# Kernel optimization log

Hardware: AMD Instinct MI355X
Metric: run time of the kernel (lower is better)

Reference implementation:

```python
import jax, jax.numpy as jnp
import numpy as np

_EPS = 1e-5
RC = 5.0   # cutoff radius
L = 20     # number of radial basis functions
N = 10000  # nodes
E = 100000 # edges
F = 128    # in_feats


def _ssp(x):
    # ShiftedSoftplus: softplus(x) - log(2)
    return jax.nn.softplus(x) - jnp.log(2.0)


def _rbf(r):
    # DimeNet radial basis: sqrt(2/rc) * sin(n*pi*r/rc) / r, n = 1..L.  r: [E,1] -> [E,L]
    n = jnp.arange(1, L + 1, dtype=r.dtype)
    return jnp.sqrt(2.0 / RC) * jnp.sin(n * jnp.pi * r / RC) / r


def _fc(u):
    # cosine cutoff applied elementwise: 0.5*(cos(pi*u/rc)+1) for u < rc else 0
    return jnp.where(u < RC, 0.5 * (jnp.cos(jnp.pi * u / RC) + 1.0), 0.0)


def setup_inputs() -> dict:
    key = jax.random.key(0)
    ks = jax.random.split(key, 12)

    def nrm(k, shape, scale=1.0):
        return jax.random.normal(k, shape, dtype=jnp.float32) * scale

    return {
        "x": nrm(ks[0], (N, 3)) * 3.0,           # atomic positions
        "v": nrm(ks[1], (N, F, 3)),               # vector node features
        "s": nrm(ks[2], (N, F)),                  # scalar node features
        "ms1_w": nrm(ks[3], (F, F), F ** -0.5),
        "ms1_b": jnp.zeros((F,), jnp.float32),
        "ms2_w": nrm(ks[4], (3 * F, F), F ** -0.5),
        "ms2_b": jnp.zeros((3 * F,), jnp.float32),
        "mv_w": nrm(ks[5], (3 * F, L), L ** -0.5),
        "mv_b": jnp.zeros((3 * F,), jnp.float32),
        "us1_w": nrm(ks[6], (F, F), F ** -0.5),
        "us1_b": jnp.zeros((F,), jnp.float32),
        "us2_w": nrm(ks[7], (3 * F, F), F ** -0.5),
        "us2_b": jnp.zeros((3 * F,), jnp.float32),
        "src": jax.random.randint(ks[8], (E,), 0, N, dtype=jnp.int32),
        "dst": jax.random.randint(ks[9], (E,), 0, N, dtype=jnp.int32),
    }


def reference(x, v, s, ms1_w, ms1_b, ms2_w, ms2_b, mv_w, mv_b,
              us1_w, us1_b, us2_w, us2_b, src, dst):
    # ---------- pass 1: message1 + reduce1 (sum over incoming edges) ----------
    sj = s[src]                                   # [E,F]   src scalar features
    vj = v[src]                                   # [E,F,3] src vector features
    vec = x[src] - x[dst]                         # [E,3]   x_i - x_j (molecule branch)
    r = jnp.sqrt(jnp.sum(vec ** 2, axis=-1) + _EPS)[:, None]          # [E,1]
    phi = _ssp(sj @ ms1_w.T + ms1_b) @ ms2_w.T + ms2_b                 # [E,3F]
    w = _fc(_rbf(r) @ mv_w.T + mv_b)                                    # [E,3F]
    v_, s_, r_ = jnp.split(phi * w, 3, axis=-1)                         # each [E,F]
    dv_e = vj * v_[:, :, None] + r_[:, :, None] * (vec / r)[:, None, :] # [E,F,3]
    dv = jax.ops.segment_sum(dv_e, dst, num_segments=N)                 # [N,F,3]
    ds = jax.ops.segment_sum(s_, dst, num_segments=N)                   # [N,F]
    v_new = v + dv
    s_new = s + ds

    # ---------- pass 2: message2 + reduce2 (mean over incoming edges) ----------
    s2 = _ssp(s_new[src] @ us1_w.T + us1_b) @ us2_w.T + us2_b           # [E,3F]
    deg = jax.ops.segment_sum(jnp.ones((E,), s.dtype), dst, num_segments=N)
    denom = jnp.maximum(deg, 1.0)
    s_mean = jax.ops.segment_sum(s2, dst, num_segments=N) / denom[:, None]        # [N,3F]
    uv = jax.ops.segment_sum(v_new[src], dst, num_segments=N) / denom[:, None, None]  # [N,F,3]
    avv, asv, ass = jnp.split(s_mean, 3, axis=-1)                       # each [N,F]
    norm = jnp.sqrt(jnp.sum(uv ** 2, axis=-1) + _EPS)[..., None]        # [N,F,1]
    dv2 = uv * avv[:, :, None]                                           # [N,F,3]
    ds2 = jnp.sum((uv / norm) ** 2, axis=-1) * asv + ass                 # [N,F]
    return (v_new + dv2, s_new + ds2)
```

## Files before the change

### kernel.cpp

```cpp
#include <hip/hip_runtime.h>
#include <hip/hip_bf16.h>


#define F_DIM   128
#define F3_DIM  384
#define L_DIM   20
#define CAP     64
#define BATCH   16

typedef __attribute__((ext_vector_type(8))) short short8;
typedef __attribute__((ext_vector_type(4))) float f32x4;
typedef __attribute__((ext_vector_type(4))) unsigned short us4;

struct u3 { unsigned a, b, c; };

__device__ __forceinline__ unsigned short f2bf(float f) {
  union { float f; unsigned u; } a; a.f = f;
  unsigned u = a.u;
  u = (u + 0x7FFFu + ((u >> 16) & 1u)) >> 16;
  return (unsigned short)u;
}
__device__ __forceinline__ float bf2f(unsigned short u) {
  union { unsigned u; float f; } a; a.u = ((unsigned)u) << 16;
  return a.f;
}

__global__ __launch_bounds__(256) void cast_fill_kernel(
    const float* __restrict__ ms1_w, unsigned short* __restrict__ w_ms1,
    const float* __restrict__ ms2_w, unsigned short* __restrict__ w_ms2,
    const float* __restrict__ us1_w, unsigned short* __restrict__ w_us1,
    const float* __restrict__ us2_w, unsigned short* __restrict__ w_us2,
    const float* __restrict__ s,     unsigned short* __restrict__ sbf,
    const float* __restrict__ v,     us4* __restrict__ v4,
    const float* __restrict__ mv_w,  unsigned short* __restrict__ mvwB,
    const int* __restrict__ src, const int* __restrict__ dst,
    int* __restrict__ cursor, int* __restrict__ jbuf,
    unsigned short* __restrict__ c1pad, unsigned short* __restrict__ c2pad,
    int nF, int E)
{
  int i = blockIdx.x * 256 + threadIdx.x;
  if (i < 16384) w_ms1[i] = f2bf(ms1_w[i]);
  if (i < 49152) w_ms2[i] = f2bf(ms2_w[i]);
  if (i < 16384) w_us1[i] = f2bf(us1_w[i]);
  if (i < 49152) w_us2[i] = f2bf(us2_w[i]);
  if (i < nF)    sbf[i] = f2bf(s[i]);
  if (i < nF) {
    const float* vp = v + (size_t)i * 3;
    us4 o; o.x = f2bf(vp[0]); o.y = f2bf(vp[1]); o.z = f2bf(vp[2]); o.w = 0;
    v4[i] = o;
  }
  if (i < 384 * 32) {
    int o = i >> 5, k = i & 31;
    float val = (k < 20) ? mv_w[o * 20 + k] * 0.6324555320336759f : 0.f;
    mvwB[i] = f2bf(val);
  }
  if (i < 768) {
    c1pad[i] = 0;
    c2pad[i] = 0;
  }
  if (i < E) {
    int d = dst[i];
    int p = atomicAdd(&cursor[d], 1);
    if (p < CAP) jbuf[d * CAP + p] = src[i];
  }
}

__global__ __launch_bounds__(512) void mlp_kernel(
    const unsigned short* __restrict__ X,
    const unsigned short* __restrict__ W1,
    const float* __restrict__ B1,
    const unsigned short* __restrict__ W2,
    const float* __restrict__ B2,
    const us4* __restrict__ Vin,
    unsigned short* __restrict__ Yc)
{
  __shared__ float HT[128 * 17];
  const int lane = threadIdx.x & 63;
  const int wave = threadIdx.x >> 6;
  const int c    = lane & 15;
  const int quad = lane >> 4;
  const int m0   = blockIdx.x * 16;

  f32x4 acc = (f32x4){0.f, 0.f, 0.f, 0.f};
#pragma unroll
  for (int kk = 0; kk < 4; kk++) {
    short8 a = *(const short8*)(X + (size_t)(m0 + c) * 128 + kk * 32 + quad * 8);
    short8 b = *(const short8*)(W1 + (size_t)(wave * 16 + c) * 128 + kk * 32 + quad * 8);
    acc = __builtin_amdgcn_mfma_f32_16x16x32_bf16(a, b, acc, 0, 0, 0);
  }
  {
    int k = wave * 16 + c;
    float bias = B1[k];
#pragma unroll
    for (int r = 0; r < 4; r++) {
      float h = acc[r] + bias;
      float sp = (h > 15.f) ? h : log1pf(__expf(h));
      sp -= 0.69314718056f;
      HT[k * 17 + quad * 4 + r] = sp;
    }
  }
  __syncthreads();

  f32x4 acc2[3];
#pragma unroll
  for (int g = 0; g < 3; g++) acc2[g] = (f32x4){0.f, 0.f, 0.f, 0.f};
#pragma unroll
  for (int kk = 0; kk < 4; kk++) {
    short8 afr;
#pragma unroll
    for (int j = 0; j < 8; j++) {
      float hv = HT[(kk * 32 + quad * 8 + j) * 17 + c];
      afr[j] = (short)f2bf(hv);
    }
#pragma unroll
    for (int g = 0; g < 3; g++) {
      short8 b = *(const short8*)(W2 + (size_t)(g * 128 + wave * 16 + c) * 128 + kk * 32 + quad * 8);
      acc2[g] = __builtin_amdgcn_mfma_f32_16x16x32_bf16(afr, b, acc2[g], 0, 0, 0);
    }
  }
  {
    int f = wave * 16 + c;
    float b0 = B2[f], b1 = B2[128 + f], b2 = B2[256 + f];
#pragma unroll
    for (int r = 0; r < 4; r++) {
      int m = quad * 4 + r;
      us4 vv = Vin[(size_t)(m0 + m) * 128 + f];
      unsigned p0 = f2bf(acc2[0][r] + b0);
      unsigned p1 = f2bf(acc2[1][r] + b1);
      unsigned p2 = f2bf(acc2[2][r] + b2);
      u3 rec;
      rec.a = p0 | (p1 << 16);
      rec.b = p2 | ((unsigned)vv.x << 16);
      rec.c = (unsigned)vv.y | ((unsigned)vv.z << 16);
      *(u3*)(Yc + ((size_t)(m0 + m) * 128 + f) * 6) = rec;
    }
  }
}

__global__ __launch_bounds__(256, 4) void pass1_kernel(
    const float* __restrict__ x,
    const unsigned short* __restrict__ combo1,
    const float* __restrict__ v,
    const float* __restrict__ s,
    const unsigned short* __restrict__ mvwB,
    const float* __restrict__ mv_b,
    const int* __restrict__ jbuf,
    const int* __restrict__ deg,
    float* __restrict__ vnew, us4* __restrict__ vnew4,
    float* __restrict__ snew, unsigned short* __restrict__ snew_bf, int nNodes)
{
  __shared__ unsigned short Asn[BATCH * 32];
  __shared__ float4 Au[BATCH];
  __shared__ us4 Wl[BATCH * 128];
  __shared__ float red[512];

  const int tid  = threadIdx.x;
  const int wave = tid >> 6, lane = tid & 63;
  const int half = wave >> 1, split = wave & 1;
  const int i = blockIdx.x;
  const int f = lane + 64 * half;
  const int c = lane & 15, quad = lane >> 4;

  int cnt = deg[i]; if (cnt > CAP) cnt = CAP;
  const int base = i * CAP;

  short8 bfr[6]; float bias[6];
#pragma unroll
  for (int p = 0; p < 3; p++)
#pragma unroll
    for (int h = 0; h < 2; h++) {
      int t = 2 * wave + h + 8 * p;
      bfr[p * 2 + h]  = *(const short8*)(mvwB + (size_t)(t * 16 + c) * 32 + quad * 8);
      bias[p * 2 + h] = mv_b[t * 16 + c];
    }

  const float xi0 = x[i * 3], xi1 = x[i * 3 + 1], xi2 = x[i * 3 + 2];
  int jv = (lane < cnt) ? jbuf[base + lane] : nNodes;

  float accV0 = 0.f, accV1 = 0.f, accV2 = 0.f, accS = 0.f;

  for (int bs = 0; bs < cnt; bs += BATCH) {
    int bcnt = cnt - bs; if (bcnt > BATCH) bcnt = BATCH;
    __syncthreads();

    if (wave == 0) {
      int t16 = lane & (BATCH - 1);
      int e = bs + t16;
      int j = __shfl(jv, e);
      if (lane < BATCH) {
        if (e < cnt) {
          float d0 = x[j * 3]     - xi0;
          float d1 = x[j * 3 + 1] - xi1;
          float d2 = x[j * 3 + 2] - xi2;
          float r = sqrtf(d0 * d0 + d1 * d1 + d2 * d2 + 1e-5f);
          float invr = 1.0f / r;
          Au[lane] = make_float4(d0 * invr, d1 * invr, d2 * invr, invr);
          float theta = r * 0.6283185307179586f;
          float s1, c1;
          __sincosf(theta, &s1, &c1);
          float c2 = 2.f * c1;
          float pm2 = s1, pm1 = c2 * s1;
          Asn[lane * 32 + 0] = f2bf(pm2);
          Asn[lane * 32 + 1] = f2bf(pm1);
#pragma unroll
          for (int l = 2; l < L_DIM; l++) {
            float cur = c2 * pm1 - pm2;
            Asn[lane * 32 + l] = f2bf(cur);
            pm2 = pm1; pm1 = cur;
          }
#pragma unroll
          for (int l = L_DIM; l < 32; l++) Asn[lane * 32 + l] = 0;
        } else {
          Au[lane] = make_float4(0.f, 0.f, 0.f, 0.f);
#pragma unroll
          for (int l = 0; l < 32; l++) Asn[lane * 32 + l] = 0;
        }
      }
    }
    __syncthreads();

    {
      short8 a = *(const short8*)&Asn[c * 32 + quad * 8];
      f32x4 acc[6];
#pragma unroll
      for (int q = 0; q < 6; q++)
        acc[q] = __builtin_amdgcn_mfma_f32_16x16x32_bf16(
            a, bfr[q], (f32x4){0.f, 0.f, 0.f, 0.f}, 0, 0, 0);
#pragma unroll
      for (int r = 0; r < 4; r++) {
        int el = quad * 4 + r;
        if (el < bcnt) {
          float invr = Au[el].w;
#pragma unroll
          for (int h = 0; h < 2; h++) {
            float wp0 = fmaf(acc[h][r],     invr, bias[h]);
            float wp1 = fmaf(acc[2 + h][r], invr, bias[2 + h]);
            float wp2 = fmaf(acc[4 + h][r], invr, bias[4 + h]);
            float w0 = (wp0 < 5.f) ? 0.5f * (__cosf(wp0 * 0.6283185307179586f) + 1.f) : 0.f;
            float w1 = (wp1 < 5.f) ? 0.5f * (__cosf(wp1 * 0.6283185307179586f) + 1.f) : 0.f;
            float w2 = (wp2 < 5.f) ? 0.5f * (__cosf(wp2 * 0.6283185307179586f) + 1.f) : 0.f;
            us4 o; o.x = f2bf(w0); o.y = f2bf(w1); o.z = f2bf(w2); o.w = 0;
            Wl[el * 128 + wave * 32 + h * 16 + c] = o;
          }
        } else {
          us4 z; z.x = 0; z.y = 0; z.z = 0; z.w = 0;
          Wl[el * 128 + wave * 32 + c]      = z;
          Wl[el * 128 + wave * 32 + 16 + c] = z;
        }
      }
    }
    __syncthreads();

    u3 cb[8];
#pragma unroll
    for (int k = 0; k < 8; k++) {
      int j = __shfl(jv, bs + split + 2 * k);
      cb[k] = *(const u3*)(combo1 + ((size_t)j * 128 + f) * 6);
    }
#pragma unroll
    for (int k = 0; k < 8; k++) {
      int el = split + 2 * k;
      float4 u = Au[el];
      us4 wv = Wl[el * 128 + f];
      float ph0 = bf2f((unsigned short)(cb[k].a & 0xffff));
      float ph1 = bf2f((unsigned short)(cb[k].a >> 16));
      float ph2 = bf2f((unsigned short)(cb[k].b & 0xffff));
      float vx  = bf2f((unsigned short)(cb[k].b >> 16));
      float vy  = bf2f((unsigned short)(cb[k].c & 0xffff));
      float vz  = bf2f((unsigned short)(cb[k].c >> 16));
      float m0 = ph0 * bf2f(wv.x);
      float m1 = ph1 * bf2f(wv.y);
      float m2 = ph2 * bf2f(wv.z);
      accV0 = fmaf(vx, m0, fmaf(m2, u.x, accV0));
      accV1 = fmaf(vy, m0, fmaf(m2, u.y, accV1));
      accV2 = fmaf(vz, m0, fmaf(m2, u.z, accV2));
      accS += m1;
    }
  }

  const int idx = half * 64 + lane;
  __syncthreads();
  if (split == 1) {
    red[idx * 4 + 0] = accV0; red[idx * 4 + 1] = accV1;
    red[idx * 4 + 2] = accV2; red[idx * 4 + 3] = accS;
  }
  __syncthreads();
  if (split == 0) {
    accV0 += red[idx * 4 + 0]; accV1 += red[idx * 4 + 1];
    accV2 += red[idx * 4 + 2]; accS  += red[idx * 4 + 3];
    size_t b3 = (size_t)i * 384 + f * 3;
    float n0 = v[b3] + accV0, n1 = v[b3 + 1] + accV1, n2 = v[b3 + 2] + accV2;
    vnew[b3] = n0; vnew[b3 + 1] = n1; vnew[b3 + 2] = n2;
    us4 o; o.x = f2bf(n0); o.y = f2bf(n1); o.z = f2bf(n2); o.w = 0;
    vnew4[(size_t)i * 128 + f] = o;
    size_t b1 = (size_t)i * 128 + f;
    float sv = s[b1] + accS;
    snew[b1] = sv;
    snew_bf[b1] = f2bf(sv);
  }
}

__global__ __launch_bounds__(256, 4) void pass2_kernel(
    const float* __restrict__ vnew,
    const float* __restrict__ snew,
    const unsigned short* __restrict__ combo2,
    const int* __restrict__ jbuf, const int* __restrict__ deg,
    float* __restrict__ vout, float* __restrict__ sout, int nNodes)
{
  __shared__ float red[1024];
  const int wave = threadIdx.x >> 6, lane = threadIdx.x & 63;
  const int half = wave >> 1, split = wave & 1;
  const int i = blockIdx.x;
  const int f = lane + 64 * half;

  int cnt = deg[i]; if (cnt > CAP) cnt = CAP;
  const int base = i * CAP;
  int jv = (lane < cnt) ? jbuf[base + lane] : nNodes;

  float accU0 = 0.f, accU1 = 0.f, accU2 = 0.f;
  float accM0 = 0.f, accM1 = 0.f, accM2 = 0.f;

  for (int b0 = split; b0 < cnt; b0 += 16) {
    u3 cb[8];
#pragma unroll
    for (int k = 0; k < 8; k++) {
      int e = b0 + 2 * k;
      int ec = (e < 63) ? e : 63;
      int j = __shfl(jv, ec);
      cb[k] = *(const u3*)(combo2 + ((size_t)j * 128 + f) * 6);
    }
#pragma unroll
    for (int k = 0; k < 8; k++) {
      accM0 += bf2f((unsigned short)(cb[k].a & 0xffff));
      accM1 += bf2f((unsigned short)(cb[k].a >> 16));
      accM2 += bf2f((unsigned short)(cb[k].b & 0xffff));
      accU0 += bf2f((unsigned short)(cb[k].b >> 16));
      accU1 += bf2f((unsigned short)(cb[k].c & 0xffff));
      accU2 += bf2f((unsigned short)(cb[k].c >> 16));
    }
  }

  const int idx = half * 64 + lane;
  if (split == 1) {
    red[idx * 8 + 0] = accU0; red[idx * 8 + 1] = accU1; red[idx * 8 + 2] = accU2;
    red[idx * 8 + 3] = accM0; red[idx * 8 + 4] = accM1; red[idx * 8 + 5] = accM2;
  }
  __syncthreads();
  if (split == 0) {
    accU0 += red[idx * 8 + 0]; accU1 += red[idx * 8 + 1]; accU2 += red[idx * 8 + 2];
    accM0 += red[idx * 8 + 3]; accM1 += red[idx * 8 + 4]; accM2 += red[idx * 8 + 5];

    float dinv = 1.0f / (float)(cnt > 0 ? cnt : 1);
    float uv0 = accU0 * dinv, uv1 = accU1 * dinv, uv2 = accU2 * dinv;
    float avv = accM0 * dinv, asv = accM1 * dinv, ass = accM2 * dinv;
    float q = uv0 * uv0 + uv1 * uv1 + uv2 * uv2;
    float ds2 = (q / (q + 1e-5f)) * asv + ass;
    size_t b3 = (size_t)i * 384 + f * 3;
    vout[b3]     = vnew[b3]     + uv0 * avv;
    vout[b3 + 1] = vnew[b3 + 1] + uv1 * avv;
    vout[b3 + 2] = vnew[b3 + 2] + uv2 * avv;
    size_t b1 = (size_t)i * 128 + f;
    sout[b1] = snew[b1] + ds2;
  }
}

extern "C" void kernel_launch(void* const* d_in, const int* in_sizes, int n_in,
                              void* d_out, int out_size, void* d_ws, size_t ws_size,
                              hipStream_t stream)
{
  const float* x     = (const float*)d_in[0];
  const float* v     = (const float*)d_in[1];
  const float* s     = (const float*)d_in[2];
  const float* ms1_w = (const float*)d_in[3];
  const float* ms1_b = (const float*)d_in[4];
  const float* ms2_w = (const float*)d_in[5];
  const float* ms2_b = (const float*)d_in[6];
  const float* mv_w  = (const float*)d_in[7];
  const float* mv_b  = (const float*)d_in[8];
  const float* us1_w = (const float*)d_in[9];
  const float* us1_b = (const float*)d_in[10];
  const float* us2_w = (const float*)d_in[11];
  const float* us2_b = (const float*)d_in[12];
  const int*   src   = (const int*)d_in[13];
  const int*   dst   = (const int*)d_in[14];

  const int N = in_sizes[0] / 3;
  const int E = in_sizes[13];

  char* p = (char*)d_ws;
  auto alloc = [&](size_t bytes) -> void* {
    void* r = (void*)p;
    p += (bytes + 255) & ~(size_t)255;
    return r;
  };
  unsigned short* sbf   = (unsigned short*)alloc((size_t)N * 128 * 2);
  unsigned short* snbf  = (unsigned short*)alloc((size_t)N * 128 * 2);
  unsigned short* w_ms1 = (unsigned short*)alloc(16384 * 2);
  unsigned short* w_ms2 = (unsigned short*)alloc(49152 * 2);
  unsigned short* w_us1 = (unsigned short*)alloc(16384 * 2);
  unsigned short* w_us2 = (unsigned short*)alloc(49152 * 2);
  unsigned short* mvwB  = (unsigned short*)alloc(384 * 32 * 2);
  us4*   v4     = (us4*)alloc((size_t)N * 128 * 8);
  us4*   vnew4  = (us4*)alloc((size_t)N * 128 * 8);
  unsigned short* combo1 = (unsigned short*)alloc((size_t)(N + 1) * 128 * 12);
  unsigned short* combo2 = (unsigned short*)alloc((size_t)(N + 1) * 128 * 12);
  float* vnew   = (float*)alloc((size_t)N * 384 * 4);
  float* snew   = (float*)alloc((size_t)N * 128 * 4);
  int* cursor   = (int*)alloc((size_t)N * 4);
  int* jbuf     = (int*)alloc((size_t)N * CAP * 4);

  hipMemsetAsync(cursor, 0, (size_t)N * 4, stream);

  cast_fill_kernel<<<(N * 128 + 255) / 256, 256, 0, stream>>>(
      ms1_w, w_ms1, ms2_w, w_ms2, us1_w, w_us1, us2_w, w_us2,
      s, sbf, v, v4, mv_w, mvwB, src, dst, cursor, jbuf,
      combo1 + (size_t)N * 768, combo2 + (size_t)N * 768, N * 128, E);

  mlp_kernel<<<N / 16, 512, 0, stream>>>(sbf, w_ms1, ms1_b, w_ms2, ms2_b,
                                         v4, combo1);

  pass1_kernel<<<N, 256, 0, stream>>>(x, combo1, v, s, mvwB, mv_b,
                                      jbuf, cursor, vnew, vnew4, snew, snbf, N);

  mlp_kernel<<<N / 16, 512, 0, stream>>>(snbf, w_us1, us1_b, w_us2, us2_b,
                                         vnew4, combo2);

  float* vout = (float*)d_out;
  float* sout = vout + (size_t)N * 384;
  pass2_kernel<<<N, 256, 0, stream>>>(vnew, snew, combo2, jbuf, cursor,
                                      vout, sout, N);
}
```

Measured before the change: 224.9 us.

## Aggregate hidden activations before second linear layer in pass 2

The second linear layer of the pass-2 message MLP is linear, so the mean over incoming edges is taken on the softplus hidden vector and the 128->384 matmul is applied once per node instead of once per source node. The hidden value is packed into the unused fourth lane of the bf16 vnew4 record, which shrinks the per-edge gather from 12 to 8 bytes. A new final kernel runs the matmul on the averaged hidden values, masks the bias for zero-degree nodes, and applies the output update. This adds one kernel launch plus uvbuf and hmean round-trips through memory, and bf16 rounding of the averaged hidden values changes numerics slightly.

```diff
diff --git a/kernel.cpp b/kernel.cpp
--- a/kernel.cpp
+++ b/kernel.cpp
@@ -35,7 +35,7 @@
     const float* __restrict__ mv_w,  unsigned short* __restrict__ mvwB,
     const int* __restrict__ src, const int* __restrict__ dst,
     int* __restrict__ cursor, int* __restrict__ jbuf,
-    unsigned short* __restrict__ c1pad, unsigned short* __restrict__ c2pad,
+    unsigned short* __restrict__ c1pad, unsigned short* __restrict__ v4pad,
     int nF, int E)
 {
   int i = blockIdx.x * 256 + threadIdx.x;
@@ -54,10 +54,8 @@
     float val = (k < 20) ? mv_w[o * 20 + k] * 0.6324555320336759f : 0.f;
     mvwB[i] = f2bf(val);
   }
-  if (i < 768) {
-    c1pad[i] = 0;
-    c2pad[i] = 0;
-  }
+  if (i < 768) c1pad[i] = 0;
+  if (i < 512) v4pad[i] = 0;
   if (i < E) {
     int d = dst[i];
     int p = atomicAdd(&cursor[d], 1);
@@ -134,6 +132,38 @@
       rec.c = (unsigned)vv.y | ((unsigned)vv.z << 16);
       *(u3*)(Yc + ((size_t)(m0 + m) * 128 + f) * 6) = rec;
     }
+  }
+}
+
+__global__ __launch_bounds__(512) void hidden_kernel(
+    const unsigned short* __restrict__ X,
+    const unsigned short* __restrict__ W1,
+    const float* __restrict__ B1,
+    us4* __restrict__ V4)
+{
+  const int lane = threadIdx.x & 63;
+  const int wave = threadIdx.x >> 6;
+  const int c    = lane & 15;
+  const int quad = lane >> 4;
+  const int m0   = blockIdx.x * 16;
+
+  f32x4 acc = (f32x4){0.f, 0.f, 0.f, 0.f};
+#pragma unroll
+  for (int kk = 0; kk < 4; kk++) {
+    short8 a = *(const short8*)(X + (size_t)(m0 + c) * 128 + kk * 32 + quad * 8);
+    short8 b = *(const short8*)(W1 + (size_t)(wave * 16 + c) * 128 + kk * 32 + quad * 8);
+    acc = __builtin_amdgcn_mfma_f32_16x16x32_bf16(a, b, acc, 0, 0, 0);
+  }
+  int f = wave * 16 + c;
+  float bias = B1[f];
+#pragma unroll
+  for (int r = 0; r < 4; r++) {
+    int m = m0 + quad * 4 + r;
+    float h = acc[r] + bias;
+    float sp = (h > 15.f) ? h : log1pf(__expf(h));
+    sp -= 0.69314718056f;
+    unsigned short* wp = (unsigned short*)(V4 + (size_t)m * 128 + f) + 3;
+    *wp = f2bf(sp);
   }
 }
 
@@ -301,13 +331,13 @@
 }
 
 __global__ __launch_bounds__(256, 4) void pass2_kernel(
-    const float* __restrict__ vnew,
-    const float* __restrict__ snew,
-    const unsigned short* __restrict__ combo2,
+    const us4* __restrict__ vnew4,
     const int* __restrict__ jbuf, const int* __restrict__ deg,
-    float* __restrict__ vout, float* __restrict__ sout, int nNodes)
-{
-  __shared__ float red[1024];
+    float* __restrict__ uvbuf,
+    unsigned short* __restrict__ hmean,
+    int nNodes)
+{
+  __shared__ float red[512];
   const int wave = threadIdx.x >> 6, lane = threadIdx.x & 63;
   const int half = wave >> 1, split = wave & 1;
   const int i = blockIdx.x;
@@ -317,50 +347,91 @@
   const int base = i * CAP;
   int jv = (lane < cnt) ? jbuf[base + lane] : nNodes;
 
-  float accU0 = 0.f, accU1 = 0.f, accU2 = 0.f;
-  float accM0 = 0.f, accM1 = 0.f, accM2 = 0.f;
+  float accU0 = 0.f, accU1 = 0.f, accU2 = 0.f, accH = 0.f;
 
   for (int b0 = split; b0 < cnt; b0 += 16) {
-    u3 cb[8];
+    us4 cb[8];
 #pragma unroll
     for (int k = 0; k < 8; k++) {
       int e = b0 + 2 * k;
       int ec = (e < 63) ? e : 63;
       int j = __shfl(jv, ec);
-      cb[k] = *(const u3*)(combo2 + ((size_t)j * 128 + f) * 6);
+      cb[k] = vnew4[(size_t)j * 128 + f];
     }
 #pragma unroll
     for (int k = 0; k < 8; k++) {
-      accM0 += bf2f((unsigned short)(cb[k].a & 0xffff));
-      accM1 += bf2f((unsigned short)(cb[k].a >> 16));
-      accM2 += bf2f((unsigned short)(cb[k].b & 0xffff));
-      accU0 += bf2f((unsigned short)(cb[k].b >> 16));
-      accU1 += bf2f((unsigned short)(cb[k].c & 0xffff));
-      accU2 += bf2f((unsigned short)(cb[k].c >> 16));
+      accU0 += bf2f(cb[k].x);
+      accU1 += bf2f(cb[k].y);
+      accU2 += bf2f(cb[k].z);
+      accH  += bf2f(cb[k].w);
     }
   }
 
   const int idx = half * 64 + lane;
   if (split == 1) {
-    red[idx * 8 + 0] = accU0; red[idx * 8 + 1] = accU1; red[idx * 8 + 2] = accU2;
-    red[idx * 8 + 3] = accM0; red[idx * 8 + 4] = accM1; red[idx * 8 + 5] = accM2;
+    red[idx * 4 + 0] = accU0; red[idx * 4 + 1] = accU1;
+    red[idx * 4 + 2] = accU2; red[idx * 4 + 3] = accH;
   }
   __syncthreads();
   if (split == 0) {
-    accU0 += red[idx * 8 + 0]; accU1 += red[idx * 8 + 1]; accU2 += red[idx * 8 + 2];
-    accM0 += red[idx * 8 + 3]; accM1 += red[idx * 8 + 4]; accM2 += red[idx * 8 + 5];
-
+    accU0 += red[idx * 4 + 0]; accU1 += red[idx * 4 + 1];
+    accU2 += red[idx * 4 + 2]; accH  += red[idx * 4 + 3];
     float dinv = 1.0f / (float)(cnt > 0 ? cnt : 1);
-    float uv0 = accU0 * dinv, uv1 = accU1 * dinv, uv2 = accU2 * dinv;
-    float avv = accM0 * dinv, asv = accM1 * dinv, ass = accM2 * dinv;
+    size_t b3 = (size_t)i * 384 + f * 3;
+    uvbuf[b3]     = accU0 * dinv;
+    uvbuf[b3 + 1] = accU1 * dinv;
+    uvbuf[b3 + 2] = accU2 * dinv;
+    hmean[(size_t)i * 128 + f] = f2bf(accH * dinv);
+  }
+}
+
+__global__ __launch_bounds__(512) void final_kernel(
+    const unsigned short* __restrict__ Hm,
+    const unsigned short* __restrict__ W2,
+    const float* __restrict__ B2,
+    const float* __restrict__ uvbuf,
+    const float* __restrict__ vnew,
+    const float* __restrict__ snew,
+    const int* __restrict__ deg,
+    float* __restrict__ vout, float* __restrict__ sout)
+{
+  const int lane = threadIdx.x & 63;
+  const int wave = threadIdx.x >> 6;
+  const int c    = lane & 15;
+  const int quad = lane >> 4;
+  const int m0   = blockIdx.x * 16;
+
+  f32x4 acc2[3];
+#pragma unroll
+  for (int g = 0; g < 3; g++) acc2[g] = (f32x4){0.f, 0.f, 0.f, 0.f};
+#pragma unroll
+  for (int kk = 0; kk < 4; kk++) {
+    short8 a = *(const short8*)(Hm + (size_t)(m0 + c) * 128 + kk * 32 + quad * 8);
+#pragma unroll
+    for (int g = 0; g < 3; g++) {
+      short8 b = *(const short8*)(W2 + (size_t)(g * 128 + wave * 16 + c) * 128 + kk * 32 + quad * 8);
+      acc2[g] = __builtin_amdgcn_mfma_f32_16x16x32_bf16(a, b, acc2[g], 0, 0, 0);
+    }
+  }
+
+  int f = wave * 16 + c;
+  float b0 = B2[f], b1 = B2[128 + f], b2 = B2[256 + f];
+#pragma unroll
+  for (int r = 0; r < 4; r++) {
+    int m = m0 + quad * 4 + r;
+    float z = (deg[m] > 0) ? 1.f : 0.f;
+    float avv = (acc2[0][r] + b0) * z;
+    float asv = (acc2[1][r] + b1) * z;
+    float ass = (acc2[2][r] + b2) * z;
+    size_t b3 = (size_t)m * 384 + f * 3;
+    float uv0 = uvbuf[b3], uv1 = uvbuf[b3 + 1], uv2 = uvbuf[b3 + 2];
     float q = uv0 * uv0 + uv1 * uv1 + uv2 * uv2;
     float ds2 = (q / (q + 1e-5f)) * asv + ass;
-    size_t b3 = (size_t)i * 384 + f * 3;
     vout[b3]     = vnew[b3]     + uv0 * avv;
     vout[b3 + 1] = vnew[b3 + 1] + uv1 * avv;
     vout[b3 + 2] = vnew[b3 + 2] + uv2 * avv;
-    size_t b1 = (size_t)i * 128 + f;
-    sout[b1] = snew[b1] + ds2;
+    size_t b1i = (size_t)m * 128 + f;
+    sout[b1i] = snew[b1i] + ds2;
   }
 }
 
@@ -401,9 +472,10 @@
   unsigned short* w_us2 = (unsigned short*)alloc(49152 * 2);
   unsigned short* mvwB  = (unsigned short*)alloc(384 * 32 * 2);
   us4*   v4     = (us4*)alloc((size_t)N * 128 * 8);
-  us4*   vnew4  = (us4*)alloc((size_t)N * 128 * 8);
+  us4*   vnew4  = (us4*)alloc((size_t)(N + 1) * 128 * 8);
   unsigned short* combo1 = (unsigned short*)alloc((size_t)(N + 1) * 128 * 12);
-  unsigned short* combo2 = (unsigned short*)alloc((size_t)(N + 1) * 128 * 12);
+  float* uvbuf  = (float*)alloc((size_t)N * 384 * 4);
+  unsigned short* hmean = (unsigned short*)alloc((size_t)N * 128 * 2);
   float* vnew   = (float*)alloc((size_t)N * 384 * 4);
   float* snew   = (float*)alloc((size_t)N * 128 * 4);
   int* cursor   = (int*)alloc((size_t)N * 4);
@@ -414,7 +486,8 @@
   cast_fill_kernel<<<(N * 128 + 255) / 256, 256, 0, stream>>>(
       ms1_w, w_ms1, ms2_w, w_ms2, us1_w, w_us1, us2_w, w_us2,
       s, sbf, v, v4, mv_w, mvwB, src, dst, cursor, jbuf,
-      combo1 + (size_t)N * 768, combo2 + (size_t)N * 768, N * 128, E);
+      combo1 + (size_t)N * 768, (unsigned short*)(vnew4 + (size_t)N * 128),
+      N * 128, E);
 
   mlp_kernel<<<N / 16, 512, 0, stream>>>(sbf, w_ms1, ms1_b, w_ms2, ms2_b,
                                          v4, combo1);
@@ -422,11 +495,12 @@
   pass1_kernel<<<N, 256, 0, stream>>>(x, combo1, v, s, mvwB, mv_b,
                                       jbuf, cursor, vnew, vnew4, snew, snbf, N);
 
-  mlp_kernel<<<N / 16, 512, 0, stream>>>(snbf, w_us1, us1_b, w_us2, us2_b,
-                                         vnew4, combo2);
+  hidden_kernel<<<N / 16, 512, 0, stream>>>(snbf, w_us1, us1_b, vnew4);
+
+  pass2_kernel<<<N, 256, 0, stream>>>(vnew4, jbuf, cursor, uvbuf, hmean, N);
 
   float* vout = (float*)d_out;
   float* sout = vout + (size_t)N * 384;
-  pass2_kernel<<<N, 256, 0, stream>>>(vnew, snew, combo2, jbuf, cursor,
-                                      vout, sout, N);
-}
+  final_kernel<<<N / 16, 512, 0, stream>>>(hmean, w_us2, us2_b, uvbuf,
+                                           vnew, snew, cursor, vout, sout);
+}
```

After: 226.0 us. No clear change (+0.5%).

## Fuse second MLP into pass kernels using linearity of mean over second layer

Applied to the files above, without the earlier changes.

Drops the second mlp_kernel launch and the combo2 buffer. Pass1 now computes the first layer plus shifted softplus of the second MLP per node with a scalar dot product and packs it into the vnew4 record. Pass2 gathers and averages that hidden vector, then applies the second linear layer once per node instead of once per edge, since the mean commutes with the affine map. This trades per-edge matmul work and traffic for per-node scalar FMA loops that read weights from global memory. It also drops the zero-fill branches and guards the accumulation by edge count instead.

```diff
diff --git a/kernel.cpp b/kernel.cpp
--- a/kernel.cpp
+++ b/kernel.cpp
@@ -35,7 +35,7 @@
     const float* __restrict__ mv_w,  unsigned short* __restrict__ mvwB,
     const int* __restrict__ src, const int* __restrict__ dst,
     int* __restrict__ cursor, int* __restrict__ jbuf,
-    unsigned short* __restrict__ c1pad, unsigned short* __restrict__ c2pad,
+    unsigned short* __restrict__ c1pad, unsigned short* __restrict__ v4pad,
     int nF, int E)
 {
   int i = blockIdx.x * 256 + threadIdx.x;
@@ -54,10 +54,8 @@
     float val = (k < 20) ? mv_w[o * 20 + k] * 0.6324555320336759f : 0.f;
     mvwB[i] = f2bf(val);
   }
-  if (i < 768) {
-    c1pad[i] = 0;
-    c2pad[i] = 0;
-  }
+  if (i < 768) c1pad[i] = 0;
+  if (i < 512) v4pad[i] = 0;
   if (i < E) {
     int d = dst[i];
     int p = atomicAdd(&cursor[d], 1);
@@ -144,15 +142,19 @@
     const float* __restrict__ s,
     const unsigned short* __restrict__ mvwB,
     const float* __restrict__ mv_b,
+    const unsigned short* __restrict__ wu1,
+    const float* __restrict__ bu1,
     const int* __restrict__ jbuf,
     const int* __restrict__ deg,
     float* __restrict__ vnew, us4* __restrict__ vnew4,
-    float* __restrict__ snew, unsigned short* __restrict__ snew_bf, int nNodes)
+    float* __restrict__ snew, int nNodes)
 {
   __shared__ unsigned short Asn[BATCH * 32];
   __shared__ float4 Au[BATCH];
   __shared__ us4 Wl[BATCH * 128];
   __shared__ float red[512];
+  __shared__ float SN[128];
+  __shared__ float PH[128];
 
   const int tid  = threadIdx.x;
   const int wave = tid >> 6, lane = tid & 63;
@@ -187,34 +189,28 @@
       int t16 = lane & (BATCH - 1);
       int e = bs + t16;
       int j = __shfl(jv, e);
-      if (lane < BATCH) {
-        if (e < cnt) {
-          float d0 = x[j * 3]     - xi0;
-          float d1 = x[j * 3 + 1] - xi1;
-          float d2 = x[j * 3 + 2] - xi2;
-          float r = sqrtf(d0 * d0 + d1 * d1 + d2 * d2 + 1e-5f);
-          float invr = 1.0f / r;
-          Au[lane] = make_float4(d0 * invr, d1 * invr, d2 * invr, invr);
-          float theta = r * 0.6283185307179586f;
-          float s1, c1;
-          __sincosf(theta, &s1, &c1);
-          float c2 = 2.f * c1;
-          float pm2 = s1, pm1 = c2 * s1;
-          Asn[lane * 32 + 0] = f2bf(pm2);
-          Asn[lane * 32 + 1] = f2bf(pm1);
-#pragma unroll
-          for (int l = 2; l < L_DIM; l++) {
-            float cur = c2 * pm1 - pm2;
-            Asn[lane * 32 + l] = f2bf(cur);
-            pm2 = pm1; pm1 = cur;
-          }
-#pragma unroll
-          for (int l = L_DIM; l < 32; l++) Asn[lane * 32 + l] = 0;
-        } else {
-          Au[lane] = make_float4(0.f, 0.f, 0.f, 0.f);
-#pragma unroll
-          for (int l = 0; l < 32; l++) Asn[lane * 32 + l] = 0;
+      if (lane < BATCH && e < cnt) {
+        float d0 = x[j * 3]     - xi0;
+        float d1 = x[j * 3 + 1] - xi1;
+        float d2 = x[j * 3 + 2] - xi2;
+        float r = sqrtf(d0 * d0 + d1 * d1 + d2 * d2 + 1e-5f);
+        float invr = 1.0f / r;
+        Au[lane] = make_float4(d0 * invr, d1 * invr, d2 * invr, invr);
+        float theta = r * 0.6283185307179586f;
+        float s1, c1;
+        __sincosf(theta, &s1, &c1);
+        float c2 = 2.f * c1;
+        float pm2 = s1, pm1 = c2 * s1;
+        Asn[lane * 32 + 0] = f2bf(pm2);
+        Asn[lane * 32 + 1] = f2bf(pm1);
+#pragma unroll
+        for (int l = 2; l < L_DIM; l++) {
+          float cur = c2 * pm1 - pm2;
+          Asn[lane * 32 + l] = f2bf(cur);
+          pm2 = pm1; pm1 = cur;
         }
+#pragma unroll
+        for (int l = L_DIM; l < 32; l++) Asn[lane * 32 + l] = 0;
       }
     }
     __syncthreads();
@@ -242,10 +238,6 @@
             us4 o; o.x = f2bf(w0); o.y = f2bf(w1); o.z = f2bf(w2); o.w = 0;
             Wl[el * 128 + wave * 32 + h * 16 + c] = o;
           }
-        } else {
-          us4 z; z.x = 0; z.y = 0; z.z = 0; z.w = 0;
-          Wl[el * 128 + wave * 32 + c]      = z;
-          Wl[el * 128 + wave * 32 + 16 + c] = z;
         }
       }
     }
@@ -260,21 +252,23 @@
 #pragma unroll
     for (int k = 0; k < 8; k++) {
       int el = split + 2 * k;
-      float4 u = Au[el];
-      us4 wv = Wl[el * 128 + f];
-      float ph0 = bf2f((unsigned short)(cb[k].a & 0xffff));
-      float ph1 = bf2f((unsigned short)(cb[k].a >> 16));
-      float ph2 = bf2f((unsigned short)(cb[k].b & 0xffff));
-      float vx  = bf2f((unsigned short)(cb[k].b >> 16));
-      float vy  = bf2f((unsigned short)(cb[k].c & 0xffff));
-      float vz  = bf2f((unsigned short)(cb[k].c >> 16));
-      float m0 = ph0 * bf2f(wv.x);
-      float m1 = ph1 * bf2f(wv.y);
-      float m2 = ph2 * bf2f(wv.z);
-      accV0 = fmaf(vx, m0, fmaf(m2, u.x, accV0));
-      accV1 = fmaf(vy, m0, fmaf(m2, u.y, accV1));
-      accV2 = fmaf(vz, m0, fmaf(m2, u.z, accV2));
-      accS += m1;
+      if (el < bcnt) {
+        float4 u = Au[el];
+        us4 wv = Wl[el * 128 + f];
+        float ph0 = bf2f((unsigned short)(cb[k].a & 0xffff));
+        float ph1 = bf2f((unsigned short)(cb[k].a >> 16));
+        float ph2 = bf2f((unsigned short)(cb[k].b & 0xffff));
+        float vx  = bf2f((unsigned short)(cb[k].b >> 16));
+        float vy  = bf2f((unsigned short)(cb[k].c & 0xffff));
+        float vz  = bf2f((unsigned short)(cb[k].c >> 16));
+        float m0 = ph0 * bf2f(wv.x);
+        float m1 = ph1 * bf2f(wv.y);
+        float m2 = ph2 * bf2f(wv.z);
+        accV0 = fmaf(vx, m0, fmaf(m2, u.x, accV0));
+        accV1 = fmaf(vy, m0, fmaf(m2, u.y, accV1));
+        accV2 = fmaf(vz, m0, fmaf(m2, u.z, accV2));
+        accS += m1;
+      }
     }
   }
 
@@ -285,29 +279,63 @@
     red[idx * 4 + 2] = accV2; red[idx * 4 + 3] = accS;
   }
   __syncthreads();
+  float n0 = 0.f, n1 = 0.f, n2 = 0.f;
   if (split == 0) {
     accV0 += red[idx * 4 + 0]; accV1 += red[idx * 4 + 1];
     accV2 += red[idx * 4 + 2]; accS  += red[idx * 4 + 3];
     size_t b3 = (size_t)i * 384 + f * 3;
-    float n0 = v[b3] + accV0, n1 = v[b3 + 1] + accV1, n2 = v[b3 + 2] + accV2;
+    n0 = v[b3] + accV0; n1 = v[b3 + 1] + accV1; n2 = v[b3 + 2] + accV2;
     vnew[b3] = n0; vnew[b3 + 1] = n1; vnew[b3 + 2] = n2;
-    us4 o; o.x = f2bf(n0); o.y = f2bf(n1); o.z = f2bf(n2); o.w = 0;
-    vnew4[(size_t)i * 128 + f] = o;
     size_t b1 = (size_t)i * 128 + f;
     float sv = s[b1] + accS;
     snew[b1] = sv;
-    snew_bf[b1] = f2bf(sv);
+    SN[f] = bf2f(f2bf(sv));
+  }
+  __syncthreads();
+
+  float hp = 0.f;
+  {
+    const int k0 = split * 64;
+    const unsigned short* wr = wu1 + (size_t)f * 128 + k0;
+#pragma unroll
+    for (int kk = 0; kk < 8; kk++) {
+      short8 w8 = *(const short8*)(wr + kk * 8);
+      float4 sa = *(const float4*)&SN[k0 + kk * 8];
+      float4 sb = *(const float4*)&SN[k0 + kk * 8 + 4];
+      hp = fmaf(bf2f((unsigned short)w8[0]), sa.x, hp);
+      hp = fmaf(bf2f((unsigned short)w8[1]), sa.y, hp);
+      hp = fmaf(bf2f((unsigned short)w8[2]), sa.z, hp);
+      hp = fmaf(bf2f((unsigned short)w8[3]), sa.w, hp);
+      hp = fmaf(bf2f((unsigned short)w8[4]), sb.x, hp);
+      hp = fmaf(bf2f((unsigned short)w8[5]), sb.y, hp);
+      hp = fmaf(bf2f((unsigned short)w8[6]), sb.z, hp);
+      hp = fmaf(bf2f((unsigned short)w8[7]), sb.w, hp);
+    }
+  }
+  if (split == 1) PH[f] = hp;
+  __syncthreads();
+  if (split == 0) {
+    float h = hp + PH[f] + bu1[f];
+    float sp = (h > 15.f) ? h : log1pf(__expf(h));
+    sp -= 0.69314718056f;
+    us4 o; o.x = f2bf(n0); o.y = f2bf(n1); o.z = f2bf(n2); o.w = f2bf(sp);
+    vnew4[(size_t)i * 128 + f] = o;
   }
 }
 
 __global__ __launch_bounds__(256, 4) void pass2_kernel(
+    const us4* __restrict__ vnew4,
+    const int* __restrict__ jbuf, const int* __restrict__ deg,
+    const unsigned short* __restrict__ W2,
+    const float* __restrict__ B2,
     const float* __restrict__ vnew,
     const float* __restrict__ snew,
-    const unsigned short* __restrict__ combo2,
-    const int* __restrict__ jbuf, const int* __restrict__ deg,
     float* __restrict__ vout, float* __restrict__ sout, int nNodes)
 {
-  __shared__ float red[1024];
+  __shared__ float red[512];
+  __shared__ float HM[128];
+  __shared__ float PP[384];
+
   const int wave = threadIdx.x >> 6, lane = threadIdx.x & 63;
   const int half = wave >> 1, split = wave & 1;
   const int i = blockIdx.x;
@@ -317,50 +345,98 @@
   const int base = i * CAP;
   int jv = (lane < cnt) ? jbuf[base + lane] : nNodes;
 
-  float accU0 = 0.f, accU1 = 0.f, accU2 = 0.f;
-  float accM0 = 0.f, accM1 = 0.f, accM2 = 0.f;
+  float accU0 = 0.f, accU1 = 0.f, accU2 = 0.f, accH = 0.f;
 
   for (int b0 = split; b0 < cnt; b0 += 16) {
-    u3 cb[8];
+    us4 cb[8];
 #pragma unroll
     for (int k = 0; k < 8; k++) {
       int e = b0 + 2 * k;
       int ec = (e < 63) ? e : 63;
       int j = __shfl(jv, ec);
-      cb[k] = *(const u3*)(combo2 + ((size_t)j * 128 + f) * 6);
+      cb[k] = vnew4[(size_t)j * 128 + f];
     }
 #pragma unroll
     for (int k = 0; k < 8; k++) {
-      accM0 += bf2f((unsigned short)(cb[k].a & 0xffff));
-      accM1 += bf2f((unsigned short)(cb[k].a >> 16));
-      accM2 += bf2f((unsigned short)(cb[k].b & 0xffff));
-      accU0 += bf2f((unsigned short)(cb[k].b >> 16));
-      accU1 += bf2f((unsigned short)(cb[k].c & 0xffff));
-      accU2 += bf2f((unsigned short)(cb[k].c >> 16));
+      int e = b0 + 2 * k;
+      if (e < cnt) {
+        accU0 += bf2f(cb[k].x);
+        accU1 += bf2f(cb[k].y);
+        accU2 += bf2f(cb[k].z);
+        accH  += bf2f(cb[k].w);
+      }
     }
   }
 
   const int idx = half * 64 + lane;
   if (split == 1) {
-    red[idx * 8 + 0] = accU0; red[idx * 8 + 1] = accU1; red[idx * 8 + 2] = accU2;
-    red[idx * 8 + 3] = accM0; red[idx * 8 + 4] = accM1; red[idx * 8 + 5] = accM2;
-  }
-  __syncthreads();
+    red[idx * 4 + 0] = accU0; red[idx * 4 + 1] = accU1;
+    red[idx * 4 + 2] = accU2; red[idx * 4 + 3] = accH;
+  }
+  __syncthreads();
+  float uv0 = 0.f, uv1 = 0.f, uv2 = 0.f;
   if (split == 0) {
-    accU0 += red[idx * 8 + 0]; accU1 += red[idx * 8 + 1]; accU2 += red[idx * 8 + 2];
-    accM0 += red[idx * 8 + 3]; accM1 += red[idx * 8 + 4]; accM2 += red[idx * 8 + 5];
-
+    accU0 += red[idx * 4 + 0]; accU1 += red[idx * 4 + 1];
+    accU2 += red[idx * 4 + 2]; accH  += red[idx * 4 + 3];
     float dinv = 1.0f / (float)(cnt > 0 ? cnt : 1);
-    float uv0 = accU0 * dinv, uv1 = accU1 * dinv, uv2 = accU2 * dinv;
-    float avv = accM0 * dinv, asv = accM1 * dinv, ass = accM2 * dinv;
+    uv0 = accU0 * dinv; uv1 = accU1 * dinv; uv2 = accU2 * dinv;
+    HM[f] = bf2f(f2bf(accH * dinv));
+  }
+  __syncthreads();
+
+  float pa = 0.f, pb = 0.f, pc = 0.f;
+  {
+    const int k0 = split * 64;
+#pragma unroll
+    for (int kk = 0; kk < 8; kk++) {
+      short8 wa = *(const short8*)(W2 + (size_t)f * 128 + k0 + kk * 8);
+      short8 wb = *(const short8*)(W2 + (size_t)(128 + f) * 128 + k0 + kk * 8);
+      short8 wc = *(const short8*)(W2 + (size_t)(256 + f) * 128 + k0 + kk * 8);
+      float4 sa = *(const float4*)&HM[k0 + kk * 8];
+      float4 sb = *(const float4*)&HM[k0 + kk * 8 + 4];
+      float hv0 = sa.x, hv1 = sa.y, hv2 = sa.z, hv3 = sa.w;
+      float hv4 = sb.x, hv5 = sb.y, hv6 = sb.z, hv7 = sb.w;
+      pa = fmaf(bf2f((unsigned short)wa[0]), hv0, pa);
+      pa = fmaf(bf2f((unsigned short)wa[1]), hv1, pa);
+      pa = fmaf(bf2f((unsigned short)wa[2]), hv2, pa);
+      pa = fmaf(bf2f((unsigned short)wa[3]), hv3, pa);
+      pa = fmaf(bf2f((unsigned short)wa[4]), hv4, pa);
+      pa = fmaf(bf2f((unsigned short)wa[5]), hv5, pa);
+      pa = fmaf(bf2f((unsigned short)wa[6]), hv6, pa);
+      pa = fmaf(bf2f((unsigned short)wa[7]), hv7, pa);
+      pb = fmaf(bf2f((unsigned short)wb[0]), hv0, pb);
+      pb = fmaf(bf2f((unsigned short)wb[1]), hv1, pb);
+      pb = fmaf(bf2f((unsigned short)wb[2]), hv2, pb);
+      pb = fmaf(bf2f((unsigned short)wb[3]), hv3, pb);
+      pb = fmaf(bf2f((unsigned short)wb[4]), hv4, pb);
+      pb = fmaf(bf2f((unsigned short)wb[5]), hv5, pb);
+      pb = fmaf(bf2f((unsigned short)wb[6]), hv6, pb);
+      pb = fmaf(bf2f((unsigned short)wb[7]), hv7, pb);
+      pc = fmaf(bf2f((unsigned short)wc[0]), hv0, pc);
+      pc = fmaf(bf2f((unsigned short)wc[1]), hv1, pc);
+      pc = fmaf(bf2f((unsigned short)wc[2]), hv2, pc);
+      pc = fmaf(bf2f((unsigned short)wc[3]), hv3, pc);
+      pc = fmaf(bf2f((unsigned short)wc[4]), hv4, pc);
+      pc = fmaf(bf2f((unsigned short)wc[5]), hv5, pc);
+      pc = fmaf(bf2f((unsigned short)wc[6]), hv6, pc);
+      pc = fmaf(bf2f((unsigned short)wc[7]), hv7, pc);
+    }
+  }
+  if (split == 1) { PP[f] = pa; PP[128 + f] = pb; PP[256 + f] = pc; }
+  __syncthreads();
+  if (split == 0) {
+    float z = (cnt > 0) ? 1.f : 0.f;
+    float avv = (pa + PP[f]       + B2[f])       * z;
+    float asv = (pb + PP[128 + f] + B2[128 + f]) * z;
+    float ass = (pc + PP[256 + f] + B2[256 + f]) * z;
     float q = uv0 * uv0 + uv1 * uv1 + uv2 * uv2;
     float ds2 = (q / (q + 1e-5f)) * asv + ass;
     size_t b3 = (size_t)i * 384 + f * 3;
     vout[b3]     = vnew[b3]     + uv0 * avv;
     vout[b3 + 1] = vnew[b3 + 1] + uv1 * avv;
     vout[b3 + 2] = vnew[b3 + 2] + uv2 * avv;
-    size_t b1 = (size_t)i * 128 + f;
-    sout[b1] = snew[b1] + ds2;
+    size_t b1i = (size_t)i * 128 + f;
+    sout[b1i] = snew[b1i] + ds2;
   }
 }
 
@@ -394,16 +470,14 @@
     return r;
   };
   unsigned short* sbf   = (unsigned short*)alloc((size_t)N * 128 * 2);
-  unsigned short* snbf  = (unsigned short*)alloc((size_t)N * 128 * 2);
   unsigned short* w_ms1 = (unsigned short*)alloc(16384 * 2);
   unsigned short* w_ms2 = (unsigned short*)alloc(49152 * 2);
   unsigned short* w_us1 = (unsigned short*)alloc(16384 * 2);
   unsigned short* w_us2 = (unsigned short*)alloc(49152 * 2);
   unsigned short* mvwB  = (unsigned short*)alloc(384 * 32 * 2);
   us4*   v4     = (us4*)alloc((size_t)N * 128 * 8);
-  us4*   vnew4  = (us4*)alloc((size_t)N * 128 * 8);
+  us4*   vnew4  = (us4*)alloc((size_t)(N + 1) * 128 * 8);
   unsigned short* combo1 = (unsigned short*)alloc((size_t)(N + 1) * 128 * 12);
-  unsigned short* combo2 = (unsigned short*)alloc((size_t)(N + 1) * 128 * 12);
   float* vnew   = (float*)alloc((size_t)N * 384 * 4);
   float* snew   = (float*)alloc((size_t)N * 128 * 4);
   int* cursor   = (int*)alloc((size_t)N * 4);
@@ -414,19 +488,18 @@
   cast_fill_kernel<<<(N * 128 + 255) / 256, 256, 0, stream>>>(
       ms1_w, w_ms1, ms2_w, w_ms2, us1_w, w_us1, us2_w, w_us2,
       s, sbf, v, v4, mv_w, mvwB, src, dst, cursor, jbuf,
-      combo1 + (size_t)N * 768, combo2 + (size_t)N * 768, N * 128, E);
+      combo1 + (size_t)N * 768, (unsigned short*)(vnew4 + (size_t)N * 128),
+      N * 128, E);
 
   mlp_kernel<<<N / 16, 512, 0, stream>>>(sbf, w_ms1, ms1_b, w_ms2, ms2_b,
                                          v4, combo1);
 
   pass1_kernel<<<N, 256, 0, stream>>>(x, combo1, v, s, mvwB, mv_b,
-                                      jbuf, cursor, vnew, vnew4, snew, snbf, N);
-
-  mlp_kernel<<<N / 16, 512, 0, stream>>>(snbf, w_us1, us1_b, w_us2, us2_b,
-                                         vnew4, combo2);
+                                      w_us1, us1_b, jbuf, cursor,
+                                      vnew, vnew4, snew, N);
 
   float* vout = (float*)d_out;
   float* sout = vout + (size_t)N * 384;
-  pass2_kernel<<<N, 256, 0, stream>>>(vnew, snew, combo2, jbuf, cursor,
-                                      vout, sout, N);
-}
+  pass2_kernel<<<N, 256, 0, stream>>>(vnew4, jbuf, cursor, w_us2, us2_b,
+                                      vnew, snew, vout, sout, N);
+}
```

New measurement: 415.1 us. +84.6%, slower.
